# Optimization experiments

Hardware: AMD Instinct MI355X
Metric: run time of the kernel (lower is better)

## Reference

```python
import jax, jax.numpy as jnp
import numpy as np

B = 262144
T = 50000
F = 19
E = 16
H = 128
D = 64
S = 3
EPS = 1e-5


def setup_inputs() -> dict:
    key = jax.random.key(0)
    ks = jax.random.split(key, 20)
    inp = {
        'home_team': jax.random.randint(ks[0], (B,), 0, T),
        'away_team': jax.random.randint(ks[1], (B,), 0, T),
        'game_features': jax.random.normal(ks[2], (B, F), dtype=jnp.float32),
        'sport_id': jax.random.randint(ks[3], (B,), 0, S),
        # parameters
        'emb_home': jax.random.normal(ks[4], (T, E), dtype=jnp.float32) * 0.1,
        'emb_away': jax.random.normal(ks[5], (T, E), dtype=jnp.float32) * 0.1,
        'W_gf': jax.random.normal(ks[6], (F, E), dtype=jnp.float32) * 0.2,
        'b_gf': jnp.zeros((E,), dtype=jnp.float32),
        'W_sh': jax.random.normal(ks[7], (3 * E, H), dtype=jnp.float32) * 0.1,
        'b_sh': jnp.zeros((H,), dtype=jnp.float32),
        'bn_gamma': jnp.ones((H,), dtype=jnp.float32),
        'bn_beta': jnp.zeros((H,), dtype=jnp.float32),
        'bn_mean': jax.random.normal(ks[8], (H,), dtype=jnp.float32) * 0.05,
        'bn_var': jax.random.uniform(ks[9], (H,), dtype=jnp.float32, minval=0.5, maxval=1.5),
        'W_exp': jax.random.normal(ks[10], (S, H, D), dtype=jnp.float32) * 0.1,
        'b_exp': jnp.zeros((S, D), dtype=jnp.float32),
        'ln_gamma': jnp.ones((S, D), dtype=jnp.float32),
        'ln_beta': jnp.zeros((S, D), dtype=jnp.float32),
        'W_out': jax.random.normal(ks[11], (D, 1), dtype=jnp.float32) * 0.1,
        'b_out': jnp.zeros((1,), dtype=jnp.float32),
    }
    return inp


def _forward(home_team, away_team, game_features, sport_id,
             emb_home, emb_away, W_gf, b_gf, W_sh, b_sh,
             bn_gamma, bn_beta, bn_mean, bn_var,
             W_exp, b_exp, ln_gamma, ln_beta, W_out, b_out):
    he = emb_home[home_team]                                  # [B, E]
    ae = emb_away[away_team]                                  # [B, E]
    gf = jax.nn.relu(game_features @ W_gf + b_gf)             # [B, E]
    x = jnp.concatenate([he, ae, gf], axis=-1)                # [B, 3E]
    # shared_fc: Linear + BatchNorm1d (eval: running stats) + ReLU (+ Dropout noop)
    s = x @ W_sh + b_sh                                       # [B, H]
    s = (s - bn_mean) * jax.lax.rsqrt(bn_var + EPS) * bn_gamma + bn_beta
    s = jax.nn.relu(s)
    # masked expert dispatch: static loop over S=3 experts, select by sport_id
    out = jnp.zeros((s.shape[0], D), dtype=s.dtype)
    for i in range(S):
        h = s @ W_exp[i] + b_exp[i]                           # [B, D]
        m = jnp.mean(h, axis=-1, keepdims=True)
        v = jnp.mean((h - m) ** 2, axis=-1, keepdims=True)
        hn = (h - m) * jax.lax.rsqrt(v + EPS) * ln_gamma[i] + ln_beta[i]
        h = jax.nn.relu(hn)
        out = jnp.where((sport_id == i)[:, None], h, out)
    return jax.nn.sigmoid(out @ W_out + b_out)                # [B, 1]


def reference(home_team, away_team, game_features, sport_id,
              emb_home, emb_away, W_gf, b_gf, W_sh, b_sh,
              bn_gamma, bn_beta, bn_mean, bn_var,
              W_exp, b_exp, ln_gamma, ln_beta, W_out, b_out):
    return _forward(home_team, away_team, game_features, sport_id,
                    emb_home, emb_away, W_gf, b_gf, W_sh, b_sh,
                    bn_gamma, bn_beta, bn_mean, bn_var,
                    W_exp, b_exp, ln_gamma, ln_beta, W_out, b_out)
```

## Files before the change

### kernel.cpp

```cpp
#include <hip/hip_runtime.h>
#include <hip/hip_bf16.h>
#include <stdint.h>

#define DEV_INLINE __device__ __forceinline__

typedef short          short8 __attribute__((ext_vector_type(8)));
typedef unsigned short u16;
typedef unsigned short u16x8  __attribute__((ext_vector_type(8)));
typedef float          f32x4  __attribute__((ext_vector_type(4)));

constexpr float EPSV = 1e-5f;


static DEV_INLINE u16 f2bf(float f) {
    return __builtin_bit_cast(u16, __float2bfloat16(f));
}

__global__ void prep_kernel(const float* __restrict__ W_gf,
                            const float* __restrict__ W_sh, const float* __restrict__ b_sh,
                            const float* __restrict__ bn_g, const float* __restrict__ bn_b,
                            const float* __restrict__ bn_m, const float* __restrict__ bn_v,
                            const float* __restrict__ Wexp,
                            unsigned char* __restrict__ ws)
{
    const int gid = blockIdx.x * blockDim.x + threadIdx.x;
    u16*   wshF = (u16*)ws;
    u16*   wexF = (u16*)(ws + 16384);
    float* scp  = (float*)(ws + 65536);
    float* shp  = (float*)(ws + 66048);
    float* wgp  = (float*)(ws + 66560);

    if (gid < 8192) {
        const int fid = gid >> 9, l = (gid >> 3) & 63, j = gid & 7;
        const int kk = fid >> 3, nt = fid & 7;
        const int k = kk*32 + ((l >> 4) << 3) + j;
        const int c = nt*16 + (l & 15);
        wshF[gid] = f2bf((k < 48) ? W_sh[k*128 + c] : 0.f);
    } else {
        const int id = gid - 8192;
        const int fid = id >> 9, l = (id >> 3) & 63, j = id & 7;
        const int s = fid >> 4, kk = (fid >> 2) & 3, nt = fid & 3;
        const int k = kk*32 + ((l >> 4) << 3) + j;
        const int d = nt*16 + (l & 15);
        wexF[id] = f2bf(Wexp[s*8192 + k*64 + d]);
    }
    if (gid < 128) {
        const float sc = bn_g[gid] * rsqrtf(bn_v[gid] + EPSV);
        scp[gid] = sc;
        shp[gid] = (b_sh[gid] - bn_m[gid]) * sc + bn_b[gid];
    }
    if (gid < 320) {
        const int f = gid >> 4, e = gid & 15;
        wgp[gid] = (f < 19) ? W_gf[f*16 + e] : 0.f;
    }
}

#define SIDX(r,j)  (((r)<<7) + ((((j)>>3) ^ ((r)&15))<<3) + ((j)&7))

__global__ __launch_bounds__(256) void fused_kernel(
    const int*   __restrict__ home,  const int* __restrict__ away,
    const float* __restrict__ gfeat, const int* __restrict__ sport,
    const float* __restrict__ emb_h, const float* __restrict__ emb_a,
    const float* __restrict__ b_gf,
    const float* __restrict__ bexp,
    const float* __restrict__ ln_g,  const float* __restrict__ ln_b,
    const float* __restrict__ wout,  const float* __restrict__ bo,
    const unsigned char* __restrict__ ws,
    float* __restrict__ out)
{
    __shared__ __align__(16) u16 Sl[4][32 * 128];

    const int tid  = threadIdx.x;
    const int lane = tid & 63;
    const int w    = tid >> 6;
    const int llo  = lane & 15;
    const int lhi  = lane >> 4;
    const int r0w  = blockIdx.x * 128 + w * 32;

    const u16*   wshF = (const u16*)ws;
    const u16*   wexF = (const u16*)(ws + 16384);
    const float* scp  = (const float*)(ws + 65536);
    const float* shp  = (const float*)(ws + 66048);
    const float* wgp  = (const float*)(ws + 66560);

    short8 a[2][2];
    {
        const int*   idxp = (lhi < 2) ? home  : away;
        const float* tab  = (lhi < 2) ? emb_h : emb_a;
        const int    off  = (lhi & 1) * 8;
#pragma unroll
        for (int mt = 0; mt < 2; ++mt) {
            const int r = r0w + mt*16 + llo;
            const float* rp = tab + (size_t)idxp[r] * 16 + off;
            const float4 v0 = *(const float4*)rp;
            const float4 v1 = *(const float4*)(rp + 4);
            u16x8 p;
            p[0]=f2bf(v0.x); p[1]=f2bf(v0.y); p[2]=f2bf(v0.z); p[3]=f2bf(v0.w);
            p[4]=f2bf(v1.x); p[5]=f2bf(v1.y); p[6]=f2bf(v1.z); p[7]=f2bf(v1.w);
            a[mt][0] = __builtin_bit_cast(short8, p);
        }
    }
    {
        const int eo = (lhi & 1) * 8;
        const int f0 = (lhi >> 1) * 10;
        float p0[8] = {0,0,0,0,0,0,0,0}, p1[8] = {0,0,0,0,0,0,0,0};
#pragma unroll
        for (int i = 0; i < 10; ++i) {
            const int f  = f0 + i;
            const int fc = (f < 19) ? f : 18;
            const float4 w0 = *(const float4*)(wgp + f*16 + eo);
            const float4 w1 = *(const float4*)(wgp + f*16 + eo + 4);
            const float g0 = gfeat[(size_t)(r0w + llo)      * 19 + fc];
            const float g1 = gfeat[(size_t)(r0w + 16 + llo) * 19 + fc];
            p0[0]=fmaf(g0,w0.x,p0[0]); p0[1]=fmaf(g0,w0.y,p0[1]); p0[2]=fmaf(g0,w0.z,p0[2]); p0[3]=fmaf(g0,w0.w,p0[3]);
            p0[4]=fmaf(g0,w1.x,p0[4]); p0[5]=fmaf(g0,w1.y,p0[5]); p0[6]=fmaf(g0,w1.z,p0[6]); p0[7]=fmaf(g0,w1.w,p0[7]);
            p1[0]=fmaf(g1,w0.x,p1[0]); p1[1]=fmaf(g1,w0.y,p1[1]); p1[2]=fmaf(g1,w0.z,p1[2]); p1[3]=fmaf(g1,w0.w,p1[3]);
            p1[4]=fmaf(g1,w1.x,p1[4]); p1[5]=fmaf(g1,w1.y,p1[5]); p1[6]=fmaf(g1,w1.z,p1[6]); p1[7]=fmaf(g1,w1.w,p1[7]);
        }
        const float4 bg0 = *(const float4*)(b_gf + eo);
        const float4 bg1 = *(const float4*)(b_gf + eo + 4);
        const float bg[8] = {bg0.x,bg0.y,bg0.z,bg0.w,bg1.x,bg1.y,bg1.z,bg1.w};
        u16x8 q0, q1;
#pragma unroll
        for (int j = 0; j < 8; ++j) {
            const float s0 = p0[j] + __shfl_xor(p0[j], 32);
            const float s1 = p1[j] + __shfl_xor(p1[j], 32);
            q0[j] = (lhi < 2) ? f2bf(fmaxf(s0 + bg[j], 0.f)) : (u16)0;
            q1[j] = (lhi < 2) ? f2bf(fmaxf(s1 + bg[j], 0.f)) : (u16)0;
        }
        a[0][1] = __builtin_bit_cast(short8, q0);
        a[1][1] = __builtin_bit_cast(short8, q1);
    }

    u16* sl = &Sl[w][0];
#pragma unroll
    for (int nt = 0; nt < 8; ++nt) {
        const short8 b0 = *(const short8*)(wshF + (0*8 + nt)*512 + lane*8);
        const short8 b1 = *(const short8*)(wshF + (1*8 + nt)*512 + lane*8);
        f32x4 c0 = {0.f,0.f,0.f,0.f}, c1 = {0.f,0.f,0.f,0.f};
        c0 = __builtin_amdgcn_mfma_f32_16x16x32_bf16(a[0][0], b0, c0, 0, 0, 0);
        c0 = __builtin_amdgcn_mfma_f32_16x16x32_bf16(a[0][1], b1, c0, 0, 0, 0);
        c1 = __builtin_amdgcn_mfma_f32_16x16x32_bf16(a[1][0], b0, c1, 0, 0, 0);
        c1 = __builtin_amdgcn_mfma_f32_16x16x32_bf16(a[1][1], b1, c1, 0, 0, 0);
        const int col = nt*16 + llo;
        const float sc = scp[col], sh = shp[col];
#pragma unroll
        for (int e = 0; e < 4; ++e) {
            sl[SIDX(lhi*4 + e,      col)] = f2bf(fmaxf(fmaf(c0[e], sc, sh), 0.f));
            sl[SIDX(16 + lhi*4 + e, col)] = f2bf(fmaxf(fmaf(c1[e], sc, sh), 0.f));
        }
    }

    short8 af[2][4];
#pragma unroll
    for (int mt = 0; mt < 2; ++mt)
#pragma unroll
        for (int kk = 0; kk < 4; ++kk)
            af[mt][kk] = *(const short8*)&sl[SIDX(mt*16 + llo, kk*32 + lhi*8)];

    int spv[2][4];
#pragma unroll
    for (int mt = 0; mt < 2; ++mt)
#pragma unroll
        for (int e = 0; e < 4; ++e)
            spv[mt][e] = sport[r0w + mt*16 + lhi*4 + e];

    float h[2][4][4];
#pragma unroll
    for (int s = 0; s < 3; ++s) {
        f32x4 ac[2][4];
#pragma unroll
        for (int mt = 0; mt < 2; ++mt)
#pragma unroll
            for (int nt = 0; nt < 4; ++nt) ac[mt][nt] = (f32x4){0.f,0.f,0.f,0.f};
#pragma unroll
        for (int nt = 0; nt < 4; ++nt) {
#pragma unroll
            for (int kk = 0; kk < 4; ++kk) {
                const short8 b = *(const short8*)(wexF + ((s*4 + kk)*4 + nt)*512 + lane*8);
                ac[0][nt] = __builtin_amdgcn_mfma_f32_16x16x32_bf16(af[0][kk], b, ac[0][nt], 0, 0, 0);
                ac[1][nt] = __builtin_amdgcn_mfma_f32_16x16x32_bf16(af[1][kk], b, ac[1][nt], 0, 0, 0);
            }
        }
#pragma unroll
        for (int nt = 0; nt < 4; ++nt) {
            const float bb = bexp[s*64 + nt*16 + llo];
#pragma unroll
            for (int mt = 0; mt < 2; ++mt)
#pragma unroll
                for (int e = 0; e < 4; ++e) {
                    const float cand = ac[mt][nt][e] + bb;
                    const bool take = (spv[mt][e] == s);
                    h[mt][nt][e] = (s == 0) ? (take ? cand : 0.f)
                                            : (take ? cand : h[mt][nt][e]);
                }
        }
    }

    float wo[4], lg0[4], lg1[4], lg2[4], lb0[4], lb1[4], lb2[4];
#pragma unroll
    for (int nt = 0; nt < 4; ++nt) {
        const int col = nt*16 + llo;
        wo[nt]  = wout[col];
        lg0[nt] = ln_g[col];       lb0[nt] = ln_b[col];
        lg1[nt] = ln_g[64 + col];  lb1[nt] = ln_b[64 + col];
        lg2[nt] = ln_g[128 + col]; lb2[nt] = ln_b[128 + col];
    }
    const float bo0 = bo[0];

#pragma unroll
    for (int mt = 0; mt < 2; ++mt) {
#pragma unroll
        for (int e = 0; e < 4; ++e) {
            const int sp = spv[mt][e];
            float m = (h[mt][0][e] + h[mt][1][e]) + (h[mt][2][e] + h[mt][3][e]);
            m += __shfl_xor(m, 1); m += __shfl_xor(m, 2); m += __shfl_xor(m, 4); m += __shfl_xor(m, 8);
            m *= (1.0f / 64.0f);
            float vv = 0.f;
#pragma unroll
            for (int nt = 0; nt < 4; ++nt) { const float c = h[mt][nt][e] - m; vv = fmaf(c, c, vv); }
            vv += __shfl_xor(vv, 1); vv += __shfl_xor(vv, 2); vv += __shfl_xor(vv, 4); vv += __shfl_xor(vv, 8);
            const float inv = rsqrtf(vv * (1.0f / 64.0f) + EPSV);
            float z = 0.f;
#pragma unroll
            for (int nt = 0; nt < 4; ++nt) {
                const float g_ = (sp == 0) ? lg0[nt] : (sp == 1 ? lg1[nt] : lg2[nt]);
                const float b_ = (sp == 0) ? lb0[nt] : (sp == 1 ? lb1[nt] : lb2[nt]);
                float hn = fmaf((h[mt][nt][e] - m) * inv, g_, b_);
                hn = fmaxf(hn, 0.f);
                z  = fmaf(hn, wo[nt], z);
            }
            z += __shfl_xor(z, 1); z += __shfl_xor(z, 2); z += __shfl_xor(z, 4); z += __shfl_xor(z, 8);
            if (llo == 0) out[r0w + mt*16 + lhi*4 + e] = 1.0f / (1.0f + __expf(-(z + bo0)));
        }
    }
}

extern "C" void kernel_launch(void* const* d_in, const int* in_sizes, int n_in,
                              void* d_out, int out_size, void* d_ws, size_t ws_size,
                              hipStream_t stream) {
    const int*   home  = (const int*)  d_in[0];
    const int*   away  = (const int*)  d_in[1];
    const float* gf    = (const float*)d_in[2];
    const int*   sport = (const int*)  d_in[3];
    const float* emb_h = (const float*)d_in[4];
    const float* emb_a = (const float*)d_in[5];
    const float* W_gf  = (const float*)d_in[6];
    const float* b_gf  = (const float*)d_in[7];
    const float* W_sh  = (const float*)d_in[8];
    const float* b_sh  = (const float*)d_in[9];
    const float* bn_g  = (const float*)d_in[10];
    const float* bn_b  = (const float*)d_in[11];
    const float* bn_m  = (const float*)d_in[12];
    const float* bn_v  = (const float*)d_in[13];
    const float* Wexp  = (const float*)d_in[14];
    const float* bexp  = (const float*)d_in[15];
    const float* ln_g  = (const float*)d_in[16];
    const float* ln_b  = (const float*)d_in[17];
    const float* wout  = (const float*)d_in[18];
    const float* bo    = (const float*)d_in[19];
    float* out = (float*)d_out;
    unsigned char* ws = (unsigned char*)d_ws;

    const int B = in_sizes[0];

    prep_kernel<<<128, 256, 0, stream>>>(W_gf, W_sh, b_sh, bn_g, bn_b, bn_m, bn_v, Wexp, ws);
    fused_kernel<<<B / 128, 256, 0, stream>>>(home, away, gf, sport, emb_h, emb_a,
                                              b_gf, bexp, ln_g, ln_b, wout, bo, ws, out);
}
```

Baseline: 179.1 us.

## Sort rows by sport within each block to skip unused expert GEMMs

Each block counts sport ids in shared memory and builds a permutation so rows of the same sport are contiguous. Each wave then runs only the expert matmuls for the sport range its 32 rows span, rather than all three experts. The LayerNorm and output epilogue is rewritten to go through a swizzled shared-memory transpose, with one lane pair per row and LN params staged in LDS. The cost is extra syncthreads and LDS atomics, plus gathered (non-coalesced) feature loads and output stores through the permutation.

```diff
diff --git a/kernel.cpp b/kernel.cpp
--- a/kernel.cpp
+++ b/kernel.cpp
@@ -56,6 +56,7 @@
 }
 
 #define SIDX(r,j)  (((r)<<7) + ((((j)>>3) ^ ((r)&15))<<3) + ((j)&7))
+static DEV_INLINE int hswz(int rho) { return (rho & 15) ^ ((rho & 8) >> 1); }
 
 __global__ __launch_bounds__(256) void fused_kernel(
     const int*   __restrict__ home,  const int* __restrict__ away,
@@ -68,14 +69,17 @@
     const unsigned char* __restrict__ ws,
     float* __restrict__ out)
 {
-    __shared__ __align__(16) u16 Sl[4][32 * 128];
+    __shared__ int cntS[3], curS[3], baseS[2];
+    __shared__ unsigned short prm[128];
+    __shared__ float lnGl[192], lnBl[192], wol[64];
+    __shared__ __align__(16) unsigned char shb[4][8192];
 
     const int tid  = threadIdx.x;
     const int lane = tid & 63;
     const int w    = tid >> 6;
     const int llo  = lane & 15;
     const int lhi  = lane >> 4;
-    const int r0w  = blockIdx.x * 128 + w * 32;
+    const int r0   = blockIdx.x * 128;
 
     const u16*   wshF = (const u16*)ws;
     const u16*   wexF = (const u16*)(ws + 16384);
@@ -83,6 +87,37 @@
     const float* shp  = (const float*)(ws + 66048);
     const float* wgp  = (const float*)(ws + 66560);
 
+    if (tid < 3) { cntS[tid] = 0; curS[tid] = 0; }
+    __syncthreads();
+    int mysp = 0;
+    if (tid < 128) {
+        mysp = sport[r0 + tid];
+        atomicAdd(&cntS[mysp], 1);
+    } else {
+        for (int i = tid - 128; i < 448; i += 128) {
+            if (i < 192)      lnGl[i]       = ln_g[i];
+            else if (i < 384) lnBl[i - 192] = ln_b[i - 192];
+            else              wol[i - 384]  = wout[i - 384];
+        }
+    }
+    __syncthreads();
+    if (tid == 0) { baseS[0] = cntS[0]; baseS[1] = cntS[0] + cntS[1]; }
+    __syncthreads();
+    if (tid < 128) {
+        const int base = (mysp == 0) ? 0 : ((mysp == 1) ? baseS[0] : baseS[1]);
+        prm[base + atomicAdd(&curS[mysp], 1)] = (unsigned short)tid;
+    }
+    __syncthreads();
+
+    const int b1 = baseS[0], b2 = baseS[1];
+    const int posW = w * 32;
+    const int spF = __builtin_amdgcn_readfirstlane((posW      >= b1) + (posW      >= b2));
+    const int spL = __builtin_amdgcn_readfirstlane((posW + 31 >= b1) + (posW + 31 >= b2));
+
+    const int pr0 = prm[posW + llo];
+    const int pr1 = prm[posW + 16 + llo];
+    const int rA0 = r0 + pr0, rA1 = r0 + pr1;
+
     short8 a[2][2];
     {
         const int*   idxp = (lhi < 2) ? home  : away;
@@ -90,7 +125,7 @@
         const int    off  = (lhi & 1) * 8;
 #pragma unroll
         for (int mt = 0; mt < 2; ++mt) {
-            const int r = r0w + mt*16 + llo;
+            const int r = mt ? rA1 : rA0;
             const float* rp = tab + (size_t)idxp[r] * 16 + off;
             const float4 v0 = *(const float4*)rp;
             const float4 v1 = *(const float4*)(rp + 4);
@@ -110,8 +145,8 @@
             const int fc = (f < 19) ? f : 18;
             const float4 w0 = *(const float4*)(wgp + f*16 + eo);
             const float4 w1 = *(const float4*)(wgp + f*16 + eo + 4);
-            const float g0 = gfeat[(size_t)(r0w + llo)      * 19 + fc];
-            const float g1 = gfeat[(size_t)(r0w + 16 + llo) * 19 + fc];
+            const float g0 = gfeat[(size_t)rA0 * 19 + fc];
+            const float g1 = gfeat[(size_t)rA1 * 19 + fc];
             p0[0]=fmaf(g0,w0.x,p0[0]); p0[1]=fmaf(g0,w0.y,p0[1]); p0[2]=fmaf(g0,w0.z,p0[2]); p0[3]=fmaf(g0,w0.w,p0[3]);
             p0[4]=fmaf(g0,w1.x,p0[4]); p0[5]=fmaf(g0,w1.y,p0[5]); p0[6]=fmaf(g0,w1.z,p0[6]); p0[7]=fmaf(g0,w1.w,p0[7]);
             p1[0]=fmaf(g1,w0.x,p1[0]); p1[1]=fmaf(g1,w0.y,p1[1]); p1[2]=fmaf(g1,w0.z,p1[2]); p1[3]=fmaf(g1,w0.w,p1[3]);
@@ -132,16 +167,16 @@
         a[1][1] = __builtin_bit_cast(short8, q1);
     }
 
-    u16* sl = &Sl[w][0];
+    u16* sl = (u16*)shb[w];
 #pragma unroll
     for (int nt = 0; nt < 8; ++nt) {
-        const short8 b0 = *(const short8*)(wshF + (0*8 + nt)*512 + lane*8);
-        const short8 b1 = *(const short8*)(wshF + (1*8 + nt)*512 + lane*8);
+        const short8 b0  = *(const short8*)(wshF + (0*8 + nt)*512 + lane*8);
+        const short8 b1f = *(const short8*)(wshF + (1*8 + nt)*512 + lane*8);
         f32x4 c0 = {0.f,0.f,0.f,0.f}, c1 = {0.f,0.f,0.f,0.f};
-        c0 = __builtin_amdgcn_mfma_f32_16x16x32_bf16(a[0][0], b0, c0, 0, 0, 0);
-        c0 = __builtin_amdgcn_mfma_f32_16x16x32_bf16(a[0][1], b1, c0, 0, 0, 0);
-        c1 = __builtin_amdgcn_mfma_f32_16x16x32_bf16(a[1][0], b0, c1, 0, 0, 0);
-        c1 = __builtin_amdgcn_mfma_f32_16x16x32_bf16(a[1][1], b1, c1, 0, 0, 0);
+        c0 = __builtin_amdgcn_mfma_f32_16x16x32_bf16(a[0][0], b0,  c0, 0, 0, 0);
+        c0 = __builtin_amdgcn_mfma_f32_16x16x32_bf16(a[0][1], b1f, c0, 0, 0, 0);
+        c1 = __builtin_amdgcn_mfma_f32_16x16x32_bf16(a[1][0], b0,  c1, 0, 0, 0);
+        c1 = __builtin_amdgcn_mfma_f32_16x16x32_bf16(a[1][1], b1f, c1, 0, 0, 0);
         const int col = nt*16 + llo;
         const float sc = scp[col], sh = shp[col];
 #pragma unroll
@@ -158,16 +193,19 @@
         for (int kk = 0; kk < 4; ++kk)
             af[mt][kk] = *(const short8*)&sl[SIDX(mt*16 + llo, kk*32 + lhi*8)];
 
-    int spv[2][4];
+    int spr[2][4];
 #pragma unroll
     for (int mt = 0; mt < 2; ++mt)
 #pragma unroll
-        for (int e = 0; e < 4; ++e)
-            spv[mt][e] = sport[r0w + mt*16 + lhi*4 + e];
-
-    float h[2][4][4];
+        for (int e = 0; e < 4; ++e) {
+            const int pos = posW + mt*16 + lhi*4 + e;
+            spr[mt][e] = (pos >= b1) + (pos >= b2);
+        }
+
+    float h[2][4][4] = {};
 #pragma unroll
     for (int s = 0; s < 3; ++s) {
+        if (s < spF || s > spL) continue;
         f32x4 ac[2][4];
 #pragma unroll
         for (int mt = 0; mt < 2; ++mt)
@@ -190,48 +228,66 @@
 #pragma unroll
                 for (int e = 0; e < 4; ++e) {
                     const float cand = ac[mt][nt][e] + bb;
-                    const bool take = (spv[mt][e] == s);
-                    h[mt][nt][e] = (s == 0) ? (take ? cand : 0.f)
-                                            : (take ? cand : h[mt][nt][e]);
+                    h[mt][nt][e] = (spr[mt][e] == s) ? cand : h[mt][nt][e];
                 }
         }
     }
 
-    float wo[4], lg0[4], lg1[4], lg2[4], lb0[4], lb1[4], lb2[4];
-#pragma unroll
-    for (int nt = 0; nt < 4; ++nt) {
-        const int col = nt*16 + llo;
-        wo[nt]  = wout[col];
-        lg0[nt] = ln_g[col];       lb0[nt] = ln_b[col];
-        lg1[nt] = ln_g[64 + col];  lb1[nt] = ln_b[64 + col];
-        lg2[nt] = ln_g[128 + col]; lb2[nt] = ln_b[128 + col];
-    }
-    const float bo0 = bo[0];
-
-#pragma unroll
-    for (int mt = 0; mt < 2; ++mt) {
-#pragma unroll
-        for (int e = 0; e < 4; ++e) {
-            const int sp = spv[mt][e];
-            float m = (h[mt][0][e] + h[mt][1][e]) + (h[mt][2][e] + h[mt][3][e]);
-            m += __shfl_xor(m, 1); m += __shfl_xor(m, 2); m += __shfl_xor(m, 4); m += __shfl_xor(m, 8);
-            m *= (1.0f / 64.0f);
-            float vv = 0.f;
-#pragma unroll
-            for (int nt = 0; nt < 4; ++nt) { const float c = h[mt][nt][e] - m; vv = fmaf(c, c, vv); }
-            vv += __shfl_xor(vv, 1); vv += __shfl_xor(vv, 2); vv += __shfl_xor(vv, 4); vv += __shfl_xor(vv, 8);
-            const float inv = rsqrtf(vv * (1.0f / 64.0f) + EPSV);
-            float z = 0.f;
-#pragma unroll
-            for (int nt = 0; nt < 4; ++nt) {
-                const float g_ = (sp == 0) ? lg0[nt] : (sp == 1 ? lg1[nt] : lg2[nt]);
-                const float b_ = (sp == 0) ? lb0[nt] : (sp == 1 ? lb1[nt] : lb2[nt]);
-                float hn = fmaf((h[mt][nt][e] - m) * inv, g_, b_);
-                hn = fmaxf(hn, 0.f);
-                z  = fmaf(hn, wo[nt], z);
+    float* hb = (float*)shb[w];
+#pragma unroll
+    for (int mt = 0; mt < 2; ++mt)
+#pragma unroll
+        for (int nt = 0; nt < 4; ++nt)
+#pragma unroll
+            for (int e = 0; e < 4; ++e) {
+                const int rho  = mt*16 + lhi*4 + e;
+                const int sraw = nt*4 + (llo >> 2);
+                const int slot = sraw ^ hswz(rho);
+                hb[rho*64 + slot*4 + (llo & 3)] = h[mt][nt][e];
             }
-            z += __shfl_xor(z, 1); z += __shfl_xor(z, 2); z += __shfl_xor(z, 4); z += __shfl_xor(z, 8);
-            if (llo == 0) out[r0w + mt*16 + lhi*4 + e] = 1.0f / (1.0f + __expf(-(z + bo0)));
+
+    {
+        const int rho = lane & 31, hf = lane >> 5;
+        float v[32];
+#pragma unroll
+        for (int j2 = 0; j2 < 8; ++j2) {
+            const int j = hf*8 + j2;
+            const int slot = j ^ hswz(rho);
+            const float4 q = *(const float4*)&hb[rho*64 + slot*4];
+            v[j2*4+0]=q.x; v[j2*4+1]=q.y; v[j2*4+2]=q.z; v[j2*4+3]=q.w;
+        }
+        float sm = 0.f;
+#pragma unroll
+        for (int i = 0; i < 32; ++i) sm += v[i];
+        sm += __shfl_xor(sm, 32);
+        const float m = sm * (1.0f / 64.0f);
+        float vv = 0.f;
+#pragma unroll
+        for (int i = 0; i < 32; ++i) { const float c = v[i] - m; vv = fmaf(c, c, vv); }
+        vv += __shfl_xor(vv, 32);
+        const float inv = rsqrtf(vv * (1.0f / 64.0f) + EPSV);
+
+        const int pos = posW + rho;
+        const int sp  = (pos >= b1) + (pos >= b2);
+        const float* lg = lnGl + sp*64 + hf*32;
+        const float* lb = lnBl + sp*64 + hf*32;
+        const float* wo = wol  + hf*32;
+        float z = 0.f;
+#pragma unroll
+        for (int q2 = 0; q2 < 8; ++q2) {
+            const float4 g4 = *(const float4*)(lg + q2*4);
+            const float4 b4 = *(const float4*)(lb + q2*4);
+            const float4 w4 = *(const float4*)(wo + q2*4);
+            float hn;
+            hn = fmaxf(fmaf((v[q2*4+0]-m)*inv, g4.x, b4.x), 0.f); z = fmaf(hn, w4.x, z);
+            hn = fmaxf(fmaf((v[q2*4+1]-m)*inv, g4.y, b4.y), 0.f); z = fmaf(hn, w4.y, z);
+            hn = fmaxf(fmaf((v[q2*4+2]-m)*inv, g4.z, b4.z), 0.f); z = fmaf(hn, w4.z, z);
+            hn = fmaxf(fmaf((v[q2*4+3]-m)*inv, g4.w, b4.w), 0.f); z = fmaf(hn, w4.w, z);
+        }
+        z += __shfl_xor(z, 32);
+        if (hf == 0) {
+            const int rl = prm[posW + rho];
+            out[r0 + rl] = 1.0f / (1.0f + __expf(-(z + bo[0])));
         }
     }
 }
```

Result: faster. 146.1 us (-18.4%).
